# Performance work log

Measured on AMD Instinct MI355X. Metric: run time of the kernel, lower is better.

The kernel has to match this reference:

```python
import jax, jax.numpy as jnp
import numpy as np

B, T, C = 1, 2048, 2048
N_HEAD, N_KV = 32, 8
HD = C // N_HEAD            # 64
N_REP = N_HEAD // N_KV      # 4
WINDOW = 512                # sliding_window
N_GLOBAL = 16               # n_global_tokens


def setup_inputs() -> dict:
    key = jax.random.key(0)
    ks = jax.random.split(key, 5)
    x = jax.random.normal(ks[0], (B, T, C), jnp.float32)
    # standard RoPE frequency tables, shape (T, HD//2)
    inv_freq = 1.0 / (10000.0 ** (np.arange(0, HD, 2, dtype=np.float32) / HD))
    ang = np.outer(np.arange(T, dtype=np.float32), inv_freq)
    freqs_cos = jnp.asarray(np.cos(ang), jnp.float32)
    freqs_sin = jnp.asarray(np.sin(ang), jnp.float32)
    s = 0.02
    wq = jax.random.normal(ks[1], (C, C), jnp.float32) * s
    wk = jax.random.normal(ks[2], (N_KV * HD, C), jnp.float32) * s
    wv = jax.random.normal(ks[3], (N_KV * HD, C), jnp.float32) * s
    wo = jax.random.normal(ks[4], (C, C), jnp.float32) * s
    return {"x": x, "freqs_cos": freqs_cos, "freqs_sin": freqs_sin,
            "wq": wq, "wk": wk, "wv": wv, "wo": wo}


def _apply_rope(xh, fc, fs):
    # xh: (B, H, T, HD); fc/fs: (T, HD//2) broadcast over (B, H)
    xr = xh.reshape(*xh.shape[:-1], HD // 2, 2)
    x0, x1 = xr[..., 0], xr[..., 1]
    fc = fc[None, None]
    fs = fs[None, None]
    out = jnp.stack([x0 * fc - x1 * fs, x0 * fs + x1 * fc], axis=-1)
    return out.reshape(xh.shape)


def reference(x, freqs_cos, freqs_sin, wq, wk, wv, wo):
    Bx, Tx, Cx = x.shape
    q = (x @ wq.T).reshape(Bx, Tx, N_HEAD, HD).transpose(0, 2, 1, 3)   # (B,Hq,T,hd)
    k = (x @ wk.T).reshape(Bx, Tx, N_KV, HD).transpose(0, 2, 1, 3)     # (B,Hkv,T,hd)
    v = (x @ wv.T).reshape(Bx, Tx, N_KV, HD).transpose(0, 2, 1, 3)
    q = _apply_rope(q, freqs_cos, freqs_sin)
    k = _apply_rope(k, freqs_cos, freqs_sin)

    # GQA: group query heads over shared kv heads instead of repeat_kv
    qg = q.reshape(Bx, N_KV, N_REP, Tx, HD)
    scale = 1.0 / float(np.sqrt(HD))
    scores = jnp.einsum('bgrqd,bgkd->bgrqk', qg, k) * scale  # (B,G,R,T,T)

    # sliding-window causal mask with global tokens (kv_cache=None branch)
    q_pos = jnp.arange(Tx)[:, None]
    k_pos = jnp.arange(Tx)[None, :]
    mask = (k_pos <= q_pos) & (k_pos >= q_pos - (WINDOW - 1))
    mask = mask | (k_pos < N_GLOBAL)
    # note: global columns combined with causal rows always leave >=1 valid key
    scores = jnp.where(mask[None, None, None], scores, -jnp.inf)
    probs = jax.nn.softmax(scores, axis=-1)

    y = jnp.einsum('bgrqk,bgkd->bgrqd', probs, v)
    y = y.reshape(Bx, N_HEAD, Tx, HD).transpose(0, 2, 1, 3).reshape(Bx, Tx, Cx)
    return y @ wo.T  # dropout p=0 in eval
```

## Files before the change

### kernel.cpp

```cpp
#include <hip/hip_runtime.h>
#include <hip/hip_bf16.h>

using short4v = __attribute__((ext_vector_type(4))) short;
using short8 = __attribute__((ext_vector_type(8))) short;
using f32x4  = __attribute__((ext_vector_type(4))) float;
using f32x16 = __attribute__((ext_vector_type(16))) float;
using int4v  = __attribute__((ext_vector_type(4))) int;

#define T_SEQ  2048
#define C_DIM  2048
#define NH     32
#define NKV    8
#define HD     64
#define WINDOW 512
#define NGLOB  16

__device__ inline ushort f2bf(float f) {
  union { float f; unsigned u; } v; v.f = f;
  unsigned u = v.u;
  u += 0x7fffu + ((u >> 16) & 1u);
  return (ushort)(u >> 16);
}
__device__ inline float bf2f(ushort h) {
  union { unsigned u; float f; } v; v.u = ((unsigned)h) << 16;
  return v.f;
}
__device__ inline float max3f(float a, float b, float c) { return fmaxf(fmaxf(a, b), c); }

__device__ __forceinline__ void gl_lds16(const ushort* g, ushort* l) {
  __builtin_amdgcn_global_load_lds(
      (const __attribute__((address_space(1))) void*)g,
      (__attribute__((address_space(3))) void*)l, 16, 0, 0);
}

__device__ __forceinline__ f32x16 zero16() {
  f32x16 v;
#pragma unroll
  for (int i = 0; i < 16; i++) v[i] = 0.f;
  return v;
}

__global__ void cvt_all(const float* __restrict__ s0, ushort* __restrict__ d0, int n0,
                        const float* __restrict__ s1, ushort* __restrict__ d1, int n1,
                        const float* __restrict__ s2, ushort* __restrict__ d2, int n2,
                        const float* __restrict__ s3, ushort* __restrict__ d3, int n3,
                        const float* __restrict__ s4, ushort* __restrict__ d4, int n4) {
  int total = n0 + n1 + n2 + n3 + n4;
  int stride = gridDim.x * blockDim.x;
  for (int i = blockIdx.x * blockDim.x + threadIdx.x; i < total; i += stride) {
    int j = i; const float* s; ushort* d;
    if (j < n0) { s = s0; d = d0; }
    else { j -= n0;
      if (j < n1) { s = s1; d = d1; }
      else { j -= n1;
        if (j < n2) { s = s2; d = d2; }
        else { j -= n2;
          if (j < n3) { s = s3; d = d3; }
          else { j -= n3; s = s4; d = d4; } } } }
    f32x4 a = *reinterpret_cast<const f32x4*>(s + (size_t)j * 8);
    f32x4 b = *reinterpret_cast<const f32x4*>(s + (size_t)j * 8 + 4);
    short8 o;
#pragma unroll
    for (int k = 0; k < 4; k++) { o[k] = (short)f2bf(a[k]); o[4 + k] = (short)f2bf(b[k]); }
    *reinterpret_cast<short8*>(d + (size_t)j * 8) = o;
  }
}

template <int MODE>
__global__ __launch_bounds__(256) void gemm2p(const ushort* __restrict__ A,
                                              const ushort* __restrict__ B0,
                                              const ushort* __restrict__ B1,
                                              const ushort* __restrict__ B2,
                                              void* __restrict__ C0,
                                              void* __restrict__ C1,
                                              void* __restrict__ C2,
                                              int K) {
  __shared__ ushort As[2][2][128][32];
  __shared__ ushort Bs[2][2][64][32];
  const int tid  = threadIdx.x;
  const int lane = tid & 63;
  const int wid  = tid >> 6;
  const int wr = wid >> 1, wc = wid & 1;
  const int r16 = lane & 15, g16 = (lane >> 4) & 3;
  const int bx = blockIdx.x, by = blockIdx.y;

  const ushort* Brow;
  void* Cout;
  int ldc, col0;
  bool vtr = false;
  if constexpr (MODE == 1) {
    if (bx < 32)      { Brow = B0 + (size_t)bx * 64 * K;        Cout = C0; ldc = 2048; col0 = bx * 64; }
    else if (bx < 40) { Brow = B1 + (size_t)(bx - 32) * 64 * K; Cout = C1; ldc = 512;  col0 = (bx - 32) * 64; }
    else              { Brow = B2 + (size_t)(bx - 40) * 64 * K; Cout = C2; ldc = 512;  col0 = (bx - 40) * 64; vtr = true; }
  } else {
    Brow = B0 + (size_t)bx * 64 * K; Cout = C0; ldc = 2048; col0 = bx * 64;
  }
  const ushort* Arow = A + (size_t)by * 128 * K;

  f32x4 acc[4][2];
#pragma unroll
  for (int i = 0; i < 4; i++)
#pragma unroll
    for (int j = 0; j < 2; j++) acc[i][j] = (f32x4){0.f, 0.f, 0.f, 0.f};

  const int srow = tid >> 2, scch = tid & 3;
  const int ssc  = scch ^ ((srow >> 1) & 3);
  const int rchunk = (g16 ^ ((r16 >> 1) & 3)) * 8;

  const int nt = K >> 6;
  int d = 0;

#define STAGE(dd, k0)                                                               \
  {                                                                                 \
    gl_lds16(&Arow[(size_t)srow * K + (k0) + ssc * 8],           &As[dd][0][srow][scch * 8]);      \
    gl_lds16(&Arow[(size_t)(srow + 64) * K + (k0) + ssc * 8],    &As[dd][0][srow + 64][scch * 8]); \
    gl_lds16(&Arow[(size_t)srow * K + (k0) + 32 + ssc * 8],      &As[dd][1][srow][scch * 8]);      \
    gl_lds16(&Arow[(size_t)(srow + 64) * K + (k0) + 32 + ssc * 8], &As[dd][1][srow + 64][scch * 8]); \
    gl_lds16(&Brow[(size_t)srow * K + (k0) + ssc * 8],           &Bs[dd][0][srow][scch * 8]);      \
    gl_lds16(&Brow[(size_t)srow * K + (k0) + 32 + ssc * 8],      &Bs[dd][1][srow][scch * 8]);      \
  }

  STAGE(0, 0);
  asm volatile("s_waitcnt vmcnt(0)" ::: "memory");
  __builtin_amdgcn_s_barrier();

  for (int t = 0; t < nt; ++t) {
    if (t + 1 < nt) {
      STAGE(d ^ 1, (t + 1) * 64);
      asm volatile("s_waitcnt vmcnt(6)" ::: "memory");
    } else {
      asm volatile("s_waitcnt vmcnt(0)" ::: "memory");
    }
    __builtin_amdgcn_s_barrier();
#pragma unroll
    for (int kk = 0; kk < 2; kk++) {
      short8 af[4], bfv[2];
#pragma unroll
      for (int i = 0; i < 4; i++)
        af[i] = *reinterpret_cast<const short8*>(&As[d][kk][wr * 64 + i * 16 + r16][rchunk]);
#pragma unroll
      for (int j = 0; j < 2; j++)
        bfv[j] = *reinterpret_cast<const short8*>(&Bs[d][kk][wc * 32 + j * 16 + r16][rchunk]);
#pragma unroll
      for (int i = 0; i < 4; i++)
#pragma unroll
        for (int j = 0; j < 2; j++)
          acc[i][j] = __builtin_amdgcn_mfma_f32_16x16x32_bf16(af[i], bfv[j], acc[i][j], 0, 0, 0);
    }
    asm volatile("" ::: "memory");
    __builtin_amdgcn_s_barrier();
    d ^= 1;
  }
#undef STAGE

#pragma unroll
  for (int i = 0; i < 4; i++)
#pragma unroll
    for (int j = 0; j < 2; j++) {
      int col = col0 + wc * 32 + j * 16 + r16;
      int row0 = by * 128 + wr * 64 + i * 16 + g16 * 4;
      if (MODE == 1 && vtr) {
        short4v tv;
#pragma unroll
        for (int r = 0; r < 4; r++) tv[r] = (short)f2bf(acc[i][j][r]);
        *reinterpret_cast<short4v*>(&((ushort*)Cout)[(size_t)col * T_SEQ + row0]) = tv;
      } else {
#pragma unroll
        for (int r = 0; r < 4; r++) {
          if constexpr (MODE == 0) ((float*)Cout)[(size_t)(row0 + r) * ldc + col] = acc[i][j][r];
          else                     ((ushort*)Cout)[(size_t)(row0 + r) * ldc + col] = f2bf(acc[i][j][r]);
        }
      }
    }
}

__global__ void rope2(ushort* __restrict__ Qb, ushort* __restrict__ Kb,
                      const float* __restrict__ fc, const float* __restrict__ fs) {
  int idx = blockIdx.x * blockDim.x + threadIdx.x;
  const int QN = T_SEQ * NH * 8;
  ushort* X; int t, hh, c, ld; float ksc;
  if (idx < QN) { X = Qb; c = idx & 7; hh = (idx >> 3) & 31; t = idx >> 8; ld = NH * HD;
                  ksc = 0.125f * 1.44269504089f; }
  else { idx -= QN; X = Kb; c = idx & 7; hh = (idx >> 3) & 7; t = idx >> 6; ld = NKV * HD;
         ksc = 1.0f; }
  size_t base = (size_t)t * ld + hh * HD + c * 8;
  short8 v = *reinterpret_cast<const short8*>(&X[base]);
  f32x4 cc = *reinterpret_cast<const f32x4*>(&fc[t * 32 + c * 4]);
  f32x4 ss = *reinterpret_cast<const f32x4*>(&fs[t * 32 + c * 4]);
  short8 o;
#pragma unroll
  for (int j = 0; j < 4; j++) {
    float x0 = bf2f((ushort)v[2 * j]), x1 = bf2f((ushort)v[2 * j + 1]);
    o[2 * j]     = (short)f2bf((x0 * cc[j] - x1 * ss[j]) * ksc);
    o[2 * j + 1] = (short)f2bf((x0 * ss[j] + x1 * cc[j]) * ksc);
  }
  *reinterpret_cast<short8*>(&X[base]) = o;
}

__global__ __launch_bounds__(512) void attn32(const ushort* __restrict__ Q,
                                              const ushort* __restrict__ K,
                                              const ushort* __restrict__ Vt,
                                              ushort* __restrict__ Y) {
  __shared__ ushort Klds[2][2][2048];
  __shared__ ushort Vlds[2][2][2048];
  __shared__ float oS[4][64][33];
  __shared__ float mS[4][32];
  __shared__ float sS[4][64];
  ushort (*Ot)[32][72] = reinterpret_cast<ushort (*)[32][72]>(&oS[0][0][0]);
  const int tid  = threadIdx.x;
  const int lane = tid & 63;
  const int wv   = tid >> 6;
  const int hh   = wv & 3;
  const int split = wv >> 2;
  const int g  = blockIdx.x & 7;
  const int qt = 63 - (blockIdx.x >> 3);
  const int h  = g * 4 + hh;
  const int q0 = qt << 5;
  const int l31 = lane & 31, hi = lane >> 5;
  const int hi8 = hi << 3, hi4 = hi << 2;
  const int qrow = q0 + l31;

  short8 qf[4];
#pragma unroll
  for (int s = 0; s < 4; s++)
    qf[s] = *reinterpret_cast<const short8*>(&Q[(size_t)qrow * C_DIM + h * HD + s * 16 + hi8]);

  f32x16 o[2] = { zero16(), zero16() };
  f32x16 sacc = zero16();
  float mrow = -1e30f;
  short8 ones8;
#pragma unroll
  for (int s = 0; s < 8; s++) ones8[s] = (short)0x3F80;

  auto pack8 = [&](const float* pp) -> short8 {
    unsigned wA, wB, wC, wD;
    asm("v_cvt_pk_bf16_f32 %0, %1, %2" : "=v"(wA) : "v"(pp[0]), "v"(pp[1]));
    asm("v_cvt_pk_bf16_f32 %0, %1, %2" : "=v"(wB) : "v"(pp[2]), "v"(pp[3]));
    asm("v_cvt_pk_bf16_f32 %0, %1, %2" : "=v"(wC) : "v"(pp[4]), "v"(pp[5]));
    asm("v_cvt_pk_bf16_f32 %0, %1, %2" : "=v"(wD) : "v"(pp[6]), "v"(pp[7]));
    asm("v_permlane32_swap_b32 %0, %1" : "+v"(wA), "+v"(wC));
    asm("v_permlane32_swap_b32 %0, %1" : "+v"(wB), "+v"(wD));
    int4v w4 = { (int)wA, (int)wB, (int)wC, (int)wD };
    return __builtin_bit_cast(short8, w4);
  };

  int wsr = (q0 - (WINDOW - 1)) >> 5;
  int wstart = (wsr < 1) ? 32 : (wsr << 5);
  int ntw = (q0 >= wstart) ? (((q0 - wstart) >> 5) + 1) : 0;
  const int NT = 1 + ntw;
  const int ihalf = (NT + 1) >> 1;

#define KBOF(i) ((i) == 0 ? 0 : wstart + ((i) - 1) * 32)
#define MSK(i)  ((i) == 0 || (KBOF(i) < q0 - 480) || (KBOF(i) == q0))

  const int sp_s = tid >> 8;
  const int kr = (tid >> 3) & 31, kc = tid & 7;
  const int vr = (tid >> 2) & 63, vc = tid & 3;
  const ushort* ksrc0 = K + (size_t)kr * (NKV * HD) + g * HD + ((kc ^ (kr & 7)) * 8);
  const ushort* vsrc0 = Vt + (size_t)(g * HD + vr) * T_SEQ + ((vc ^ ((vr >> 1) & 3)) * 8);
  ushort* kdst[2] = { &Klds[sp_s][0][(tid & 255) * 8], &Klds[sp_s][1][(tid & 255) * 8] };
  ushort* vdst[2] = { &Vlds[sp_s][0][(tid & 255) * 8], &Vlds[sp_s][1][(tid & 255) * 8] };

#define STAGE(dd, i0t, i1t)                                                    \
  {                                                                            \
    int idxs = sp_s ? (i1t) : (i0t);                                           \
    if (idxs > NT - 1) idxs = NT - 1;                                          \
    int kbs = KBOF(idxs);                                                      \
    gl_lds16(ksrc0 + (size_t)kbs * (NKV * HD), kdst[dd]);                      \
    gl_lds16(vsrc0 + kbs, vdst[dd]);                                           \
  }

#define PROCESS(dd, kb, domask)                                                    \
  {                                                                                \
    short8 kf0 = *reinterpret_cast<const short8*>(                                 \
        &Klds[split][dd][l31 * 64 + (((0 * 2 + hi) ^ (l31 & 7)) * 8)]);            \
    short8 kf1 = *reinterpret_cast<const short8*>(                                 \
        &Klds[split][dd][l31 * 64 + (((1 * 2 + hi) ^ (l31 & 7)) * 8)]);            \
    short8 kf2 = *reinterpret_cast<const short8*>(                                 \
        &Klds[split][dd][l31 * 64 + (((2 * 2 + hi) ^ (l31 & 7)) * 8)]);            \
    short8 kf3 = *reinterpret_cast<const short8*>(                                 \
        &Klds[split][dd][l31 * 64 + (((3 * 2 + hi) ^ (l31 & 7)) * 8)]);            \
    f32x16 sa = zero16();                                                          \
    __builtin_amdgcn_s_setprio(1);                                                 \
    sa = __builtin_amdgcn_mfma_f32_32x32x16_bf16(kf0, qf[0], sa, 0, 0, 0);         \
    sa = __builtin_amdgcn_mfma_f32_32x32x16_bf16(kf1, qf[1], sa, 0, 0, 0);         \
    sa = __builtin_amdgcn_mfma_f32_32x32x16_bf16(kf2, qf[2], sa, 0, 0, 0);         \
    sa = __builtin_amdgcn_mfma_f32_32x32x16_bf16(kf3, qf[3], sa, 0, 0, 0);         \
    __builtin_amdgcn_s_setprio(0);                                                 \
    float p[16];                                                                   \
    _Pragma("unroll") for (int r = 0; r < 16; r++) p[r] = sa[r];                   \
    if (domask) {                                                                  \
      _Pragma("unroll") for (int r = 0; r < 16; r++) {                             \
        int kidx = (kb) + (r & 3) + 8 * (r >> 2) + hi4;                            \
        bool ok = ((kidx <= qrow) && (kidx >= qrow - (WINDOW - 1))) || (kidx < NGLOB); \
        p[r] = ok ? p[r] : -1e30f;                                                 \
      }                                                                            \
    }                                                                              \
    float m0 = max3f(p[0], p[1], p[2]);                                            \
    float m1 = max3f(p[3], p[4], p[5]);                                            \
    float m2 = max3f(p[6], p[7], p[8]);                                            \
    float m3 = max3f(p[9], p[10], p[11]);                                          \
    float m4 = max3f(p[12], p[13], p[14]);                                         \
    float tmax = fmaxf(max3f(m0, m1, m2), max3f(m3, m4, p[15]));                   \
    float pmax = fmaxf(tmax, __shfl_xor(tmax, 32));                                \
    if (!__all(pmax <= mrow + 8.0f)) {                                             \
      float mnew = fmaxf(mrow, pmax);                                              \
      float corr = exp2f(mrow - mnew);                                             \
      sacc[0] *= corr;                                                             \
      _Pragma("unroll") for (int r = 0; r < 16; r++) { o[0][r] *= corr; o[1][r] *= corr; } \
      mrow = mnew;                                                                 \
    }                                                                              \
    _Pragma("unroll") for (int r = 0; r < 16; r++) p[r] = exp2f(p[r] - mrow);      \
    short8 pb0 = pack8(&p[0]);                                                     \
    short8 pb1 = pack8(&p[8]);                                                     \
    short8 v0 = *reinterpret_cast<const short8*>(                                  \
        &Vlds[split][dd][(0 * 32 + l31) * 32 + (((0 * 2 + hi) ^ ((l31 >> 1) & 3)) * 8)]); \
    short8 v1 = *reinterpret_cast<const short8*>(                                  \
        &Vlds[split][dd][(0 * 32 + l31) * 32 + (((1 * 2 + hi) ^ ((l31 >> 1) & 3)) * 8)]); \
    short8 v2 = *reinterpret_cast<const short8*>(                                  \
        &Vlds[split][dd][(1 * 32 + l31) * 32 + (((0 * 2 + hi) ^ (((32 + l31) >> 1) & 3)) * 8)]); \
    short8 v3 = *reinterpret_cast<const short8*>(                                  \
        &Vlds[split][dd][(1 * 32 + l31) * 32 + (((1 * 2 + hi) ^ (((32 + l31) >> 1) & 3)) * 8)]); \
    __builtin_amdgcn_s_setprio(1);                                                 \
    sacc = __builtin_amdgcn_mfma_f32_32x32x16_bf16(ones8, pb0, sacc, 0, 0, 0);     \
    sacc = __builtin_amdgcn_mfma_f32_32x32x16_bf16(ones8, pb1, sacc, 0, 0, 0);     \
    o[0] = __builtin_amdgcn_mfma_f32_32x32x16_bf16(v0, pb0, o[0], 0, 0, 0);        \
    o[0] = __builtin_amdgcn_mfma_f32_32x32x16_bf16(v1, pb1, o[0], 0, 0, 0);        \
    o[1] = __builtin_amdgcn_mfma_f32_32x32x16_bf16(v2, pb0, o[1], 0, 0, 0);        \
    o[1] = __builtin_amdgcn_mfma_f32_32x32x16_bf16(v3, pb1, o[1], 0, 0, 0);        \
    __builtin_amdgcn_s_setprio(0);                                                 \
  }

  STAGE(0, 0, ihalf);
  asm volatile("s_waitcnt vmcnt(0)" ::: "memory");
  __builtin_amdgcn_s_barrier();
  int d = 0;
  for (int it = 0; it < ihalf; ++it) {
    if (it + 1 < ihalf) {
      STAGE(d ^ 1, it + 1, ihalf + it + 1);
      asm volatile("s_waitcnt vmcnt(2)" ::: "memory");
    } else {
      asm volatile("s_waitcnt vmcnt(0)" ::: "memory");
    }
    __builtin_amdgcn_s_barrier();
    int idx = split ? (ihalf + it) : it;
    if (idx < NT) {
      int kb = KBOF(idx);
      PROCESS(d, kb, MSK(idx));
    }
    asm volatile("" ::: "memory");
    __builtin_amdgcn_s_barrier();
    d ^= 1;
  }
#undef STAGE
#undef PROCESS
#undef KBOF
#undef MSK

  float ssum = sacc[0];

  if (split == 1) {
    if (hi == 0) mS[hh][l31] = mrow;
    sS[hh][lane] = ssum;
#pragma unroll
    for (int ntl = 0; ntl < 2; ntl++)
#pragma unroll
      for (int r = 0; r < 16; r++) oS[hh][lane][ntl * 16 + r] = o[ntl][r];
  }
  __syncthreads();

  float inv = 0.f;
  if (split == 0) {
    float mB = mS[hh][l31];
    float sB = sS[hh][lane];
    float mN = fmaxf(mrow, mB);
    float cA = exp2f(mrow - mN), cB = exp2f(mB - mN);
    ssum = ssum * cA + sB * cB;
#pragma unroll
    for (int ntl = 0; ntl < 2; ntl++)
#pragma unroll
      for (int r = 0; r < 16; r++)
        o[ntl][r] = o[ntl][r] * cA + oS[hh][lane][ntl * 16 + r] * cB;
    inv = 1.0f / ssum;
  }
  __syncthreads();

  if (split == 0) {
#pragma unroll
    for (int ntl = 0; ntl < 2; ntl++)
#pragma unroll
      for (int r = 0; r < 16; r++) {
        int dim = ntl * 32 + (r & 3) + 8 * (r >> 2) + hi4;
        Ot[hh][l31][dim] = f2bf(o[ntl][r] * inv);
      }
  }
  __syncthreads();

  if (split == 0) {
    int qq = lane >> 1, hf = lane & 1;
#pragma unroll
    for (int c = 0; c < 4; c++) {
      short8 vv = *reinterpret_cast<const short8*>(&Ot[hh][qq][hf * 32 + c * 8]);
      *reinterpret_cast<short8*>(&Y[(size_t)(q0 + qq) * C_DIM + h * HD + hf * 32 + c * 8]) = vv;
    }
  }
}

extern "C" void kernel_launch(void* const* d_in, const int* in_sizes, int n_in,
                              void* d_out, int out_size, void* d_ws, size_t ws_size,
                              hipStream_t stream) {
  const float* x  = (const float*)d_in[0];
  const float* fc = (const float*)d_in[1];
  const float* fs = (const float*)d_in[2];
  const float* wq = (const float*)d_in[3];
  const float* wk = (const float*)d_in[4];
  const float* wv = (const float*)d_in[5];
  const float* wo = (const float*)d_in[6];
  float* out = (float*)d_out;

  const size_t SZ_X = (size_t)T_SEQ * C_DIM;
  const size_t SZ_W = (size_t)(NKV * HD) * C_DIM;

  ushort* xb  = (ushort*)d_ws;
  ushort* wqb = xb  + SZ_X;
  ushort* wkb = wqb + SZ_X;
  ushort* wvb = wkb + SZ_W;
  ushort* wob = wvb + SZ_W;
  ushort* Qb  = wob + SZ_X;
  ushort* Kb  = Qb  + SZ_X;
  ushort* Vt  = Kb  + SZ_W;
  ushort* Yb  = Vt  + SZ_W;

  cvt_all<<<1024, 256, 0, stream>>>(x,  xb,  (int)(SZ_X / 8),
                                    wq, wqb, (int)(SZ_X / 8),
                                    wk, wkb, (int)(SZ_W / 8),
                                    wv, wvb, (int)(SZ_W / 8),
                                    wo, wob, (int)(SZ_X / 8));

  gemm2p<1><<<dim3(48, 16), 256, 0, stream>>>(xb, wqb, wkb, wvb, Qb, Kb, Vt, C_DIM);

  rope2<<<(T_SEQ * (NH + NKV) * 8) / 256, 256, 0, stream>>>(Qb, Kb, fc, fs);

  attn32<<<512, 512, 0, stream>>>(Qb, Kb, Vt, Yb);

  gemm2p<0><<<dim3(32, 16), 256, 0, stream>>>(Yb, wob, nullptr, nullptr, out, nullptr, nullptr, C_DIM);
}
```

Baseline: 119.6 us.

## Fuse weight conversion into GEMM B-loads and RoPE into QKV epilogue

The GEMM now reads fp32 weights straight from global memory into registers, converts them to bf16 with packed cvt instructions, and writes them into LDS. This removes the separate conversion pass over all four weight matrices. RoPE and the Q scaling are applied in the QKV GEMM epilogue using a lane shuffle, which drops the separate rope kernel. In exchange the GEMM reads twice the bytes for B and pays register staging and VALU conversion inside the main loop, and it now waits for all loads to finish on every iteration, which weakens the prefetch overlap.

```diff
diff --git a/kernel.cpp b/kernel.cpp
--- a/kernel.cpp
+++ b/kernel.cpp
@@ -14,6 +14,7 @@
 #define HD     64
 #define WINDOW 512
 #define NGLOB  16
+#define KLOG   0.180336880f
 
 __device__ inline ushort f2bf(float f) {
   union { float f; unsigned u; } v; v.f = f;
@@ -40,40 +41,36 @@
   return v;
 }
 
-__global__ void cvt_all(const float* __restrict__ s0, ushort* __restrict__ d0, int n0,
-                        const float* __restrict__ s1, ushort* __restrict__ d1, int n1,
-                        const float* __restrict__ s2, ushort* __restrict__ d2, int n2,
-                        const float* __restrict__ s3, ushort* __restrict__ d3, int n3,
-                        const float* __restrict__ s4, ushort* __restrict__ d4, int n4) {
-  int total = n0 + n1 + n2 + n3 + n4;
+__device__ __forceinline__ short8 cvt8(f32x4 a, f32x4 b) {
+  unsigned w0, w1, w2, w3;
+  asm("v_cvt_pk_bf16_f32 %0, %1, %2" : "=v"(w0) : "v"(a[0]), "v"(a[1]));
+  asm("v_cvt_pk_bf16_f32 %0, %1, %2" : "=v"(w1) : "v"(a[2]), "v"(a[3]));
+  asm("v_cvt_pk_bf16_f32 %0, %1, %2" : "=v"(w2) : "v"(b[0]), "v"(b[1]));
+  asm("v_cvt_pk_bf16_f32 %0, %1, %2" : "=v"(w3) : "v"(b[2]), "v"(b[3]));
+  int4v w = { (int)w0, (int)w1, (int)w2, (int)w3 };
+  return __builtin_bit_cast(short8, w);
+}
+
+__global__ void cvt_f32_bf16(const float* __restrict__ in, ushort* __restrict__ out, int n8) {
+  int i = blockIdx.x * blockDim.x + threadIdx.x;
   int stride = gridDim.x * blockDim.x;
-  for (int i = blockIdx.x * blockDim.x + threadIdx.x; i < total; i += stride) {
-    int j = i; const float* s; ushort* d;
-    if (j < n0) { s = s0; d = d0; }
-    else { j -= n0;
-      if (j < n1) { s = s1; d = d1; }
-      else { j -= n1;
-        if (j < n2) { s = s2; d = d2; }
-        else { j -= n2;
-          if (j < n3) { s = s3; d = d3; }
-          else { j -= n3; s = s4; d = d4; } } } }
-    f32x4 a = *reinterpret_cast<const f32x4*>(s + (size_t)j * 8);
-    f32x4 b = *reinterpret_cast<const f32x4*>(s + (size_t)j * 8 + 4);
-    short8 o;
-#pragma unroll
-    for (int k = 0; k < 4; k++) { o[k] = (short)f2bf(a[k]); o[4 + k] = (short)f2bf(b[k]); }
-    *reinterpret_cast<short8*>(d + (size_t)j * 8) = o;
+  for (; i < n8; i += stride) {
+    f32x4 a = *reinterpret_cast<const f32x4*>(in + (size_t)i * 8);
+    f32x4 b = *reinterpret_cast<const f32x4*>(in + (size_t)i * 8 + 4);
+    *reinterpret_cast<short8*>(out + (size_t)i * 8) = cvt8(a, b);
   }
 }
 
 template <int MODE>
 __global__ __launch_bounds__(256) void gemm2p(const ushort* __restrict__ A,
-                                              const ushort* __restrict__ B0,
-                                              const ushort* __restrict__ B1,
-                                              const ushort* __restrict__ B2,
+                                              const float* __restrict__ B0,
+                                              const float* __restrict__ B1,
+                                              const float* __restrict__ B2,
                                               void* __restrict__ C0,
                                               void* __restrict__ C1,
                                               void* __restrict__ C2,
+                                              const float* __restrict__ fc,
+                                              const float* __restrict__ fs,
                                               int K) {
   __shared__ ushort As[2][2][128][32];
   __shared__ ushort Bs[2][2][64][32];
@@ -84,7 +81,7 @@
   const int r16 = lane & 15, g16 = (lane >> 4) & 3;
   const int bx = blockIdx.x, by = blockIdx.y;
 
-  const ushort* Brow;
+  const float* Brow;
   void* Cout;
   int ldc, col0;
   bool vtr = false;
@@ -105,33 +102,40 @@
 
   const int srow = tid >> 2, scch = tid & 3;
   const int ssc  = scch ^ ((srow >> 1) & 3);
+  const int bwc  = (scch ^ ((srow >> 1) & 3)) * 8;
   const int rchunk = (g16 ^ ((r16 >> 1) & 3)) * 8;
+  const float* Bthr = Brow + (size_t)srow * K + scch * 8;
 
   const int nt = K >> 6;
   int d = 0;
-
-#define STAGE(dd, k0)                                                               \
-  {                                                                                 \
-    gl_lds16(&Arow[(size_t)srow * K + (k0) + ssc * 8],           &As[dd][0][srow][scch * 8]);      \
-    gl_lds16(&Arow[(size_t)(srow + 64) * K + (k0) + ssc * 8],    &As[dd][0][srow + 64][scch * 8]); \
-    gl_lds16(&Arow[(size_t)srow * K + (k0) + 32 + ssc * 8],      &As[dd][1][srow][scch * 8]);      \
-    gl_lds16(&Arow[(size_t)(srow + 64) * K + (k0) + 32 + ssc * 8], &As[dd][1][srow + 64][scch * 8]); \
-    gl_lds16(&Brow[(size_t)srow * K + (k0) + ssc * 8],           &Bs[dd][0][srow][scch * 8]);      \
-    gl_lds16(&Brow[(size_t)srow * K + (k0) + 32 + ssc * 8],      &Bs[dd][1][srow][scch * 8]);      \
-  }
-
-  STAGE(0, 0);
-  asm volatile("s_waitcnt vmcnt(0)" ::: "memory");
+  f32x4 vb0a, vb0b, vb1a, vb1b;
+
+#define STAGE_ISSUE(k0)                                                              \
+  {                                                                                  \
+    vb0a = *reinterpret_cast<const f32x4*>(Bthr + (k0));                             \
+    vb0b = *reinterpret_cast<const f32x4*>(Bthr + (k0) + 4);                         \
+    vb1a = *reinterpret_cast<const f32x4*>(Bthr + (k0) + 32);                        \
+    vb1b = *reinterpret_cast<const f32x4*>(Bthr + (k0) + 32 + 4);                    \
+    gl_lds16(&Arow[(size_t)srow * K + (k0) + ssc * 8],             &As[d ^ 1][0][srow][scch * 8]);      \
+    gl_lds16(&Arow[(size_t)(srow + 64) * K + (k0) + ssc * 8],      &As[d ^ 1][0][srow + 64][scch * 8]); \
+    gl_lds16(&Arow[(size_t)srow * K + (k0) + 32 + ssc * 8],        &As[d ^ 1][1][srow][scch * 8]);      \
+    gl_lds16(&Arow[(size_t)(srow + 64) * K + (k0) + 32 + ssc * 8], &As[d ^ 1][1][srow + 64][scch * 8]); \
+  }
+#define STAGE_WRITE()                                                                \
+  {                                                                                  \
+    *reinterpret_cast<short8*>(&Bs[d ^ 1][0][srow][bwc]) = cvt8(vb0a, vb0b);         \
+    *reinterpret_cast<short8*>(&Bs[d ^ 1][1][srow][bwc]) = cvt8(vb1a, vb1b);         \
+  }
+
+  d = 1;
+  STAGE_ISSUE(0);
+  STAGE_WRITE();
+  asm volatile("s_waitcnt vmcnt(0) lgkmcnt(0)" ::: "memory");
   __builtin_amdgcn_s_barrier();
+  d = 0;
 
   for (int t = 0; t < nt; ++t) {
-    if (t + 1 < nt) {
-      STAGE(d ^ 1, (t + 1) * 64);
-      asm volatile("s_waitcnt vmcnt(6)" ::: "memory");
-    } else {
-      asm volatile("s_waitcnt vmcnt(0)" ::: "memory");
-    }
-    __builtin_amdgcn_s_barrier();
+    if (t + 1 < nt) STAGE_ISSUE((t + 1) * 64);
 #pragma unroll
     for (int kk = 0; kk < 2; kk++) {
       short8 af[4], bfv[2];
@@ -147,11 +151,16 @@
         for (int j = 0; j < 2; j++)
           acc[i][j] = __builtin_amdgcn_mfma_f32_16x16x32_bf16(af[i], bfv[j], acc[i][j], 0, 0, 0);
     }
-    asm volatile("" ::: "memory");
+    if (t + 1 < nt) STAGE_WRITE();
+    asm volatile("s_waitcnt vmcnt(0) lgkmcnt(0)" ::: "memory");
     __builtin_amdgcn_s_barrier();
     d ^= 1;
   }
-#undef STAGE
+#undef STAGE_ISSUE
+#undef STAGE_WRITE
+
+  const bool doRope = (MODE == 1) && !vtr;
+  const float ksc = (MODE == 1 && bx < 32) ? KLOG : 1.0f;
 
 #pragma unroll
   for (int i = 0; i < 4; i++)
@@ -164,6 +173,18 @@
 #pragma unroll
         for (int r = 0; r < 4; r++) tv[r] = (short)f2bf(acc[i][j][r]);
         *reinterpret_cast<short4v*>(&((ushort*)Cout)[(size_t)col * T_SEQ + row0]) = tv;
+      } else if (doRope) {
+        int pr = (col & 63) >> 1;
+        bool ev = ((col & 1) == 0);
+#pragma unroll
+        for (int r = 0; r < 4; r++) {
+          float a = acc[i][j][r];
+          float b = __shfl_xor(a, 1);
+          int t = row0 + r;
+          float c = fc[t * 32 + pr], s = fs[t * 32 + pr];
+          float v = ev ? (a * c - b * s) : (b * s + a * c);
+          ((ushort*)Cout)[(size_t)t * ldc + col] = f2bf(v * ksc);
+        }
       } else {
 #pragma unroll
         for (int r = 0; r < 4; r++) {
@@ -172,29 +193,6 @@
         }
       }
     }
-}
-
-__global__ void rope2(ushort* __restrict__ Qb, ushort* __restrict__ Kb,
-                      const float* __restrict__ fc, const float* __restrict__ fs) {
-  int idx = blockIdx.x * blockDim.x + threadIdx.x;
-  const int QN = T_SEQ * NH * 8;
-  ushort* X; int t, hh, c, ld; float ksc;
-  if (idx < QN) { X = Qb; c = idx & 7; hh = (idx >> 3) & 31; t = idx >> 8; ld = NH * HD;
-                  ksc = 0.125f * 1.44269504089f; }
-  else { idx -= QN; X = Kb; c = idx & 7; hh = (idx >> 3) & 7; t = idx >> 6; ld = NKV * HD;
-         ksc = 1.0f; }
-  size_t base = (size_t)t * ld + hh * HD + c * 8;
-  short8 v = *reinterpret_cast<const short8*>(&X[base]);
-  f32x4 cc = *reinterpret_cast<const f32x4*>(&fc[t * 32 + c * 4]);
-  f32x4 ss = *reinterpret_cast<const f32x4*>(&fs[t * 32 + c * 4]);
-  short8 o;
-#pragma unroll
-  for (int j = 0; j < 4; j++) {
-    float x0 = bf2f((ushort)v[2 * j]), x1 = bf2f((ushort)v[2 * j + 1]);
-    o[2 * j]     = (short)f2bf((x0 * cc[j] - x1 * ss[j]) * ksc);
-    o[2 * j + 1] = (short)f2bf((x0 * ss[j] + x1 * cc[j]) * ksc);
-  }
-  *reinterpret_cast<short8*>(&X[base]) = o;
 }
 
 __global__ __launch_bounds__(512) void attn32(const ushort* __restrict__ Q,
@@ -422,26 +420,17 @@
   const size_t SZ_W = (size_t)(NKV * HD) * C_DIM;
 
   ushort* xb  = (ushort*)d_ws;
-  ushort* wqb = xb  + SZ_X;
-  ushort* wkb = wqb + SZ_X;
-  ushort* wvb = wkb + SZ_W;
-  ushort* wob = wvb + SZ_W;
-  ushort* Qb  = wob + SZ_X;
-  ushort* Kb  = Qb  + SZ_X;
-  ushort* Vt  = Kb  + SZ_W;
-  ushort* Yb  = Vt  + SZ_W;
-
-  cvt_all<<<1024, 256, 0, stream>>>(x,  xb,  (int)(SZ_X / 8),
-                                    wq, wqb, (int)(SZ_X / 8),
-                                    wk, wkb, (int)(SZ_W / 8),
-                                    wv, wvb, (int)(SZ_W / 8),
-                                    wo, wob, (int)(SZ_X / 8));
-
-  gemm2p<1><<<dim3(48, 16), 256, 0, stream>>>(xb, wqb, wkb, wvb, Qb, Kb, Vt, C_DIM);
-
-  rope2<<<(T_SEQ * (NH + NKV) * 8) / 256, 256, 0, stream>>>(Qb, Kb, fc, fs);
+  ushort* Qb  = xb + SZ_X;
+  ushort* Kb  = Qb + SZ_X;
+  ushort* Vt  = Kb + SZ_W;
+  ushort* Yb  = Vt + SZ_W;
+
+  cvt_f32_bf16<<<512, 256, 0, stream>>>(x, xb, (int)(SZ_X / 8));
+
+  gemm2p<1><<<dim3(48, 16), 256, 0, stream>>>(xb, wq, wk, wv, Qb, Kb, Vt, fc, fs, C_DIM);
 
   attn32<<<512, 512, 0, stream>>>(Qb, Kb, Vt, Yb);
 
-  gemm2p<0><<<dim3(32, 16), 256, 0, stream>>>(Yb, wob, nullptr, nullptr, out, nullptr, nullptr, C_DIM);
-}
+  gemm2p<0><<<dim3(32, 16), 256, 0, stream>>>(Yb, wo, nullptr, nullptr, out, nullptr, nullptr,
+                                              fc, fs, C_DIM);
+}
```

Result: no change. 121.6 us (+1.7%).
